# Optimization experiments

Hardware: AMD Instinct MI355X
Metric: run time of the kernel (lower is better)

The kernel has to match this reference:

```python
import jax, jax.numpy as jnp
import numpy as np

# Dims from init_kwargs
B, L, D = 32, 512, 1024
NSEC = 4
SSIZE = D // NSEC          # 256
LATENT = 256
N_TOKENS = 32
BANDS = ((0, 64), (16, 128), (32, 192), (64, 256))
COEF = 0.1


def _dct_mat(N):
    # torch_dct.dct (DCT-II, unnormalized, factor 2): X[k] = 2*sum_n x[n] cos(pi*k*(2n+1)/(2N))
    n = jnp.arange(N, dtype=jnp.float32)
    k = jnp.arange(N, dtype=jnp.float32)[:, None]
    return 2.0 * jnp.cos(jnp.pi * (2.0 * n + 1.0) * k / (2.0 * N))  # [k, n]


def _idct_mat(N):
    # exact inverse of the above (DCT-III form): x[n] = (1/N)*(X[0]/2 + sum_{k>=1} X[k] cos(pi*k*(2n+1)/(2N)))
    k = jnp.arange(N, dtype=jnp.float32)
    n = jnp.arange(N, dtype=jnp.float32)[:, None]
    M = jnp.cos(jnp.pi * k * (2.0 * n + 1.0) / (2.0 * N)) / N
    return M.at[:, 0].set(1.0 / (2.0 * N))  # [n, k]


def setup_inputs() -> dict:
    key = jax.random.key(0)
    k1, k2, k3 = jax.random.split(key, 3)
    encoding = jax.random.normal(k1, (B, L, D), dtype=jnp.float32)
    W = jax.random.normal(k2, (LATENT, SSIZE), dtype=jnp.float32) / np.float32(np.sqrt(SSIZE))
    b = jax.random.normal(k3, (LATENT,), dtype=jnp.float32) * 0.01
    return {"encoding": encoding, "W": W, "b": b}


def reference(encoding, W, b):
    # encoding: [B, L, D] -> [B, L, NSEC, SSIZE]
    enc = encoding.reshape(B, L, NSEC, SSIZE)
    # Literal semantics of the torch code: H = enc[:,:,i] is [B,L,S]; H.T -> [S,L,B];
    # dct/idct act over the LAST axis (= batch), scaling indexes the seq axis.
    C = _dct_mat(B)   # [k, b]
    M = _idct_mat(B)  # [b, k]
    # DCT along batch axis for all sectors at once: [k, L, NSEC, SSIZE]
    Dk = jnp.einsum('kb,blns->klns', C, enc)
    # Per-sector band scaling along the seq axis
    seq = jnp.arange(L)
    mask = jnp.stack(
        [jnp.where((seq < lo) | (seq >= hi), jnp.float32(COEF), jnp.float32(1.0)) for (lo, hi) in BANDS],
        axis=1,
    )  # [L, NSEC]
    Dk = Dk * mask[None, :, :, None]
    # IDCT back along batch axis: [B, L, NSEC, SSIZE]
    filt = jnp.einsum('bk,klns->blns', M, Dk)
    # Linear(SSIZE -> LATENT) + tanh, then keep first N_TOKENS positions
    y = jnp.tanh(jnp.einsum('blns,os->blno', filt, W) + b)
    return y[:, :N_TOKENS]
```

## Files before the change

kernel.cpp:

```cpp
#include <hip/hip_runtime.h>
#include <math.h>

#define LSEQ   512
#define DDIM   1024
#define KDIM   256
#define COLS   256
#define ROWS   4096
#define COEF   0.1f

#define TR    32
#define TC    64
#define BK    64
#define STRA  260
#define STRW  68


__device__ __forceinline__ float tanh_fast(float x) {
    return 1.0f - 2.0f / (__expf(2.0f * x) + 1.0f);
}

__global__ __launch_bounds__(256, 2)
void spectral_gemm_kernel(const float* __restrict__ enc,
                          const float* __restrict__ W,
                          const float* __restrict__ bias,
                          float* __restrict__ out) {
    __shared__ float As[TR * STRA];
    __shared__ float Ws[TC * STRW];

    const int t      = threadIdx.x;
    const int tile_r = blockIdx.x * TR;
    const int tile_c = blockIdx.y * TC;

    const float* srcA = enc + (size_t)(tile_r >> 7) * (size_t)(LSEQ * DDIM)
                            + (size_t)(tile_r & 127) * KDIM;
    #pragma unroll
    for (int it = 0; it < 8; ++it) {
        const int f  = t + it * 256;
        const int r  = f >> 6;
        const int k4 = f & 63;
        const float4 v = *(const float4*)(srcA + (size_t)f * 4);
        *(float4*)&As[r * STRA + k4 * 4] = v;
    }

    const int tx = t & 15;
    const int ty = t >> 4;
    const int r0 = 2 * ty;

    float acc[2][4] = {{0.f,0.f,0.f,0.f},{0.f,0.f,0.f,0.f}};

    for (int p = 0; p < 4; ++p) {
        const int kk = p * BK;

        #pragma unroll
        for (int it = 0; it < 4; ++it) {
            const int o  = (t >> 4) + it * 16;
            const int k4 = t & 15;
            const float4 v =
                *(const float4*)&W[(size_t)(tile_c + o) * KDIM + kk + k4 * 4];
            *(float4*)&Ws[o * STRW + k4 * 4] = v;
        }
        __syncthreads();

        #pragma unroll 8
        for (int k = 0; k < BK; k += 4) {
            const float4 a0 = *(const float4*)&As[r0 * STRA + kk + k];
            const float4 a1 = *(const float4*)&As[(r0 + 1) * STRA + kk + k];
            float4 w[4];
            #pragma unroll
            for (int c = 0; c < 4; ++c)
                w[c] = *(const float4*)&Ws[(tx + 16 * c) * STRW + k];
            #pragma unroll
            for (int c = 0; c < 4; ++c) {
                acc[0][c] += a0.x * w[c].x;
                acc[0][c] += a0.y * w[c].y;
                acc[0][c] += a0.z * w[c].z;
                acc[0][c] += a0.w * w[c].w;
                acc[1][c] += a1.x * w[c].x;
                acc[1][c] += a1.y * w[c].y;
                acc[1][c] += a1.z * w[c].z;
                acc[1][c] += a1.w * w[c].w;
            }
        }
        __syncthreads();
    }

    #pragma unroll
    for (int i = 0; i < 2; ++i) {
        const int row = tile_r + r0 + i;
        const int n = row & 3;
        const int l = (row >> 2) & 31;
        const float scale = (n == 0 || (n == 1 && l >= 16)) ? 1.0f : COEF;
        #pragma unroll
        for (int c = 0; c < 4; ++c) {
            const int col = tile_c + tx + 16 * c;
            out[(size_t)row * COLS + col] = tanh_fast(scale * acc[i][c] + bias[col]);
        }
    }
}

extern "C" void kernel_launch(void* const* d_in, const int* in_sizes, int n_in,
                              void* d_out, int out_size, void* d_ws, size_t ws_size,
                              hipStream_t stream) {
    const float* enc  = (const float*)d_in[0];
    const float* W    = (const float*)d_in[1];
    const float* bias = (const float*)d_in[2];
    float* out = (float*)d_out;

    dim3 grid(ROWS / TR, COLS / TC);
    spectral_gemm_kernel<<<grid, dim3(256), 0, stream>>>(enc, W, bias, out);
}
```

Baseline: 102.9 us.

## Replace LDS-tiled GEMM with register-streamed kernel over pre-transposed weights

Adds a small kernel that transposes W into a float4-interleaved layout in the workspace on every call. The main kernel drops shared-memory tiling: each thread owns one output column for 8 rows and streams A and W straight from global memory, with a one-step software prefetch. All threads in a wavefront read the same A address, so those loads broadcast. The goal is to remove LDS traffic and barriers, at the cost of an extra launch, more L2 reads of W per block, and a prefetch that reads one step past the end of the buffers.

```diff
diff --git a/kernel.cpp b/kernel.cpp
--- a/kernel.cpp
+++ b/kernel.cpp
@@ -8,93 +8,85 @@
 #define ROWS   4096
 #define COEF   0.1f
 
-#define TR    32
-#define TC    64
-#define BK    64
-#define STRA  260
-#define STRW  68
+#define TRB    8
 
 
 __device__ __forceinline__ float tanh_fast(float x) {
     return 1.0f - 2.0f / (__expf(2.0f * x) + 1.0f);
 }
 
+__global__ __launch_bounds__(256, 4)
+void transpose_w4_kernel(const float* __restrict__ W, float* __restrict__ Wt4) {
+    __shared__ float tile[32][33];
+    const int t  = threadIdx.x;
+    const int bx = blockIdx.x;
+    const int by = blockIdx.y;
+    #pragma unroll
+    for (int i = 0; i < 4; ++i) {
+        const int e   = t + i * 256;
+        const int o_l = e >> 5;
+        const int k_l = e & 31;
+        tile[o_l][k_l] = W[(size_t)(by * 32 + o_l) * KDIM + bx * 32 + k_l];
+    }
+    __syncthreads();
+    const int k4_l = t >> 5;
+    const int o_l  = t & 31;
+    float4 v;
+    v.x = tile[o_l][4 * k4_l + 0];
+    v.y = tile[o_l][4 * k4_l + 1];
+    v.z = tile[o_l][4 * k4_l + 2];
+    v.w = tile[o_l][4 * k4_l + 3];
+    *(float4*)&Wt4[(size_t)(bx * 8 + k4_l) * 1024 + (size_t)(by * 32 + o_l) * 4] = v;
+}
+
 __global__ __launch_bounds__(256, 2)
 void spectral_gemm_kernel(const float* __restrict__ enc,
-                          const float* __restrict__ W,
+                          const float* __restrict__ Wt4,
                           const float* __restrict__ bias,
                           float* __restrict__ out) {
-    __shared__ float As[TR * STRA];
-    __shared__ float Ws[TC * STRW];
+    const int t    = threadIdx.x;
+    const int row0 = blockIdx.x * TRB;
 
-    const int t      = threadIdx.x;
-    const int tile_r = blockIdx.x * TR;
-    const int tile_c = blockIdx.y * TC;
+    const float* __restrict__ abase = enc + (size_t)(row0 >> 7) * (size_t)(LSEQ * DDIM)
+                                          + (size_t)(row0 & 127) * KDIM;
+    const float* __restrict__ wbase = Wt4 + (size_t)t * 4;
 
-    const float* srcA = enc + (size_t)(tile_r >> 7) * (size_t)(LSEQ * DDIM)
-                            + (size_t)(tile_r & 127) * KDIM;
+    float acc[TRB] = {0.f, 0.f, 0.f, 0.f, 0.f, 0.f, 0.f, 0.f};
+
+    float4 w = *(const float4*)(wbase);
+    float4 a[TRB];
     #pragma unroll
-    for (int it = 0; it < 8; ++it) {
-        const int f  = t + it * 256;
-        const int r  = f >> 6;
-        const int k4 = f & 63;
-        const float4 v = *(const float4*)(srcA + (size_t)f * 4);
-        *(float4*)&As[r * STRA + k4 * 4] = v;
+    for (int r = 0; r < TRB; ++r)
+        a[r] = *(const float4*)(abase + r * KDIM);
+
+    #pragma unroll 4
+    for (int p = 0; p < 64; ++p) {
+        const float4 wn = *(const float4*)(wbase + (size_t)(p + 1) * 1024);
+        float4 an[TRB];
+        #pragma unroll
+        for (int r = 0; r < TRB; ++r)
+            an[r] = *(const float4*)(abase + r * KDIM + (p + 1) * 4);
+
+        #pragma unroll
+        for (int r = 0; r < TRB; ++r) {
+            acc[r] += a[r].x * w.x;
+            acc[r] += a[r].y * w.y;
+            acc[r] += a[r].z * w.z;
+            acc[r] += a[r].w * w.w;
+        }
+        w = wn;
+        #pragma unroll
+        for (int r = 0; r < TRB; ++r) a[r] = an[r];
     }
 
-    const int tx = t & 15;
-    const int ty = t >> 4;
-    const int r0 = 2 * ty;
-
-    float acc[2][4] = {{0.f,0.f,0.f,0.f},{0.f,0.f,0.f,0.f}};
-
-    for (int p = 0; p < 4; ++p) {
-        const int kk = p * BK;
-
-        #pragma unroll
-        for (int it = 0; it < 4; ++it) {
-            const int o  = (t >> 4) + it * 16;
-            const int k4 = t & 15;
-            const float4 v =
-                *(const float4*)&W[(size_t)(tile_c + o) * KDIM + kk + k4 * 4];
-            *(float4*)&Ws[o * STRW + k4 * 4] = v;
-        }
-        __syncthreads();
-
-        #pragma unroll 8
-        for (int k = 0; k < BK; k += 4) {
-            const float4 a0 = *(const float4*)&As[r0 * STRA + kk + k];
-            const float4 a1 = *(const float4*)&As[(r0 + 1) * STRA + kk + k];
-            float4 w[4];
-            #pragma unroll
-            for (int c = 0; c < 4; ++c)
-                w[c] = *(const float4*)&Ws[(tx + 16 * c) * STRW + k];
-            #pragma unroll
-            for (int c = 0; c < 4; ++c) {
-                acc[0][c] += a0.x * w[c].x;
-                acc[0][c] += a0.y * w[c].y;
-                acc[0][c] += a0.z * w[c].z;
-                acc[0][c] += a0.w * w[c].w;
-                acc[1][c] += a1.x * w[c].x;
-                acc[1][c] += a1.y * w[c].y;
-                acc[1][c] += a1.z * w[c].z;
-                acc[1][c] += a1.w * w[c].w;
-            }
-        }
-        __syncthreads();
-    }
-
+    const float b = bias[t];
     #pragma unroll
-    for (int i = 0; i < 2; ++i) {
-        const int row = tile_r + r0 + i;
+    for (int r = 0; r < TRB; ++r) {
+        const int row = row0 + r;
         const int n = row & 3;
         const int l = (row >> 2) & 31;
         const float scale = (n == 0 || (n == 1 && l >= 16)) ? 1.0f : COEF;
-        #pragma unroll
-        for (int c = 0; c < 4; ++c) {
-            const int col = tile_c + tx + 16 * c;
-            out[(size_t)row * COLS + col] = tanh_fast(scale * acc[i][c] + bias[col]);
-        }
+        out[(size_t)row * COLS + t] = tanh_fast(scale * acc[r] + b);
     }
 }
 
@@ -105,7 +97,8 @@
     const float* W    = (const float*)d_in[1];
     const float* bias = (const float*)d_in[2];
     float* out = (float*)d_out;
+    float* Wt4 = (float*)d_ws;
 
-    dim3 grid(ROWS / TR, COLS / TC);
-    spectral_gemm_kernel<<<grid, dim3(256), 0, stream>>>(enc, W, bias, out);
+    transpose_w4_kernel<<<dim3(8, 8), dim3(256), 0, stream>>>(W, Wt4);
+    spectral_gemm_kernel<<<dim3(ROWS / TRB), dim3(256), 0, stream>>>(enc, Wt4, bias, out);
 }
```

After: 131.5 us. +27.9%, slower.

## Restructure GEMM: wave-uniform W reads from global, XOR-swizzled A tile

Applied to the files above, without the earlier changes.

Changes the block tile from 32x64 to 64x32. W is no longer staged in shared memory. Each wavefront takes 8 output columns, picked wave-uniformly through readfirstlane, and reads W straight from global or cache as broadcast loads. Each lane owns one row of the A tile, which is stored with an XOR swizzle to avoid LDS bank conflicts, and the outputs are written as float4. This removes the per-chunk W staging and barriers, at the cost of a larger 64 KB LDS footprint, which may lower occupancy, and of reading the A tile twice as often relative to W across blocks.

```diff
diff --git a/kernel.cpp b/kernel.cpp
--- a/kernel.cpp
+++ b/kernel.cpp
@@ -8,11 +8,8 @@
 #define ROWS   4096
 #define COEF   0.1f
 
-#define TR    32
-#define TC    64
-#define BK    64
-#define STRA  260
-#define STRW  68
+#define TRB    64
+#define TCB    32
 
 
 __device__ __forceinline__ float tanh_fast(float x) {
@@ -24,78 +21,56 @@
                           const float* __restrict__ W,
                           const float* __restrict__ bias,
                           float* __restrict__ out) {
-    __shared__ float As[TR * STRA];
-    __shared__ float Ws[TC * STRW];
+    __shared__ float As[TRB * KDIM];
 
     const int t      = threadIdx.x;
-    const int tile_r = blockIdx.x * TR;
-    const int tile_c = blockIdx.y * TC;
+    const int tile_r = blockIdx.x * TRB;
+    const int tile_c = blockIdx.y * TCB;
 
     const float* srcA = enc + (size_t)(tile_r >> 7) * (size_t)(LSEQ * DDIM)
                             + (size_t)(tile_r & 127) * KDIM;
     #pragma unroll
-    for (int it = 0; it < 8; ++it) {
-        const int f  = t + it * 256;
+    for (int i = 0; i < 16; ++i) {
+        const int f  = t + i * 256;
         const int r  = f >> 6;
         const int k4 = f & 63;
         const float4 v = *(const float4*)(srcA + (size_t)f * 4);
-        *(float4*)&As[r * STRA + k4 * 4] = v;
+        *(float4*)&As[r * KDIM + ((k4 ^ (r & 15)) << 2)] = v;
+    }
+    __syncthreads();
+
+    const int lane = t & 63;
+    const int cg   = __builtin_amdgcn_readfirstlane(t >> 6);
+    const float* __restrict__ Wp   = W + (size_t)(tile_c + cg * 8) * KDIM;
+    const float* __restrict__ arow = As + lane * KDIM;
+    const int swz = lane & 15;
+
+    float acc[8] = {0.f,0.f,0.f,0.f,0.f,0.f,0.f,0.f};
+
+    #pragma unroll 4
+    for (int p = 0; p < 64; ++p) {
+        const float4 a = *(const float4*)(arow + ((p ^ swz) << 2));
+        #pragma unroll
+        for (int c = 0; c < 8; ++c) {
+            const float4 w = *(const float4*)(Wp + c * KDIM + p * 4);
+            acc[c] += a.x * w.x;
+            acc[c] += a.y * w.y;
+            acc[c] += a.z * w.z;
+            acc[c] += a.w * w.w;
+        }
     }
 
-    const int tx = t & 15;
-    const int ty = t >> 4;
-    const int r0 = 2 * ty;
-
-    float acc[2][4] = {{0.f,0.f,0.f,0.f},{0.f,0.f,0.f,0.f}};
-
-    for (int p = 0; p < 4; ++p) {
-        const int kk = p * BK;
-
-        #pragma unroll
-        for (int it = 0; it < 4; ++it) {
-            const int o  = (t >> 4) + it * 16;
-            const int k4 = t & 15;
-            const float4 v =
-                *(const float4*)&W[(size_t)(tile_c + o) * KDIM + kk + k4 * 4];
-            *(float4*)&Ws[o * STRW + k4 * 4] = v;
-        }
-        __syncthreads();
-
-        #pragma unroll 8
-        for (int k = 0; k < BK; k += 4) {
-            const float4 a0 = *(const float4*)&As[r0 * STRA + kk + k];
-            const float4 a1 = *(const float4*)&As[(r0 + 1) * STRA + kk + k];
-            float4 w[4];
-            #pragma unroll
-            for (int c = 0; c < 4; ++c)
-                w[c] = *(const float4*)&Ws[(tx + 16 * c) * STRW + k];
-            #pragma unroll
-            for (int c = 0; c < 4; ++c) {
-                acc[0][c] += a0.x * w[c].x;
-                acc[0][c] += a0.y * w[c].y;
-                acc[0][c] += a0.z * w[c].z;
-                acc[0][c] += a0.w * w[c].w;
-                acc[1][c] += a1.x * w[c].x;
-                acc[1][c] += a1.y * w[c].y;
-                acc[1][c] += a1.z * w[c].z;
-                acc[1][c] += a1.w * w[c].w;
-            }
-        }
-        __syncthreads();
-    }
-
+    const int row = tile_r + lane;
+    const int n = row & 3;
+    const int l = (row >> 2) & 31;
+    const float scale = (n == 0 || (n == 1 && l >= 16)) ? 1.0f : COEF;
+    float o[8];
     #pragma unroll
-    for (int i = 0; i < 2; ++i) {
-        const int row = tile_r + r0 + i;
-        const int n = row & 3;
-        const int l = (row >> 2) & 31;
-        const float scale = (n == 0 || (n == 1 && l >= 16)) ? 1.0f : COEF;
-        #pragma unroll
-        for (int c = 0; c < 4; ++c) {
-            const int col = tile_c + tx + 16 * c;
-            out[(size_t)row * COLS + col] = tanh_fast(scale * acc[i][c] + bias[col]);
-        }
-    }
+    for (int c = 0; c < 8; ++c)
+        o[c] = tanh_fast(scale * acc[c] + bias[tile_c + cg * 8 + c]);
+    float4* outp = (float4*)(out + (size_t)row * COLS + tile_c + cg * 8);
+    outp[0] = make_float4(o[0], o[1], o[2], o[3]);
+    outp[1] = make_float4(o[4], o[5], o[6], o[7]);
 }
 
 extern "C" void kernel_launch(void* const* d_in, const int* in_sizes, int n_in,
@@ -106,6 +81,6 @@
     const float* bias = (const float*)d_in[2];
     float* out = (float*)d_out;
 
-    dim3 grid(ROWS / TR, COLS / TC);
+    dim3 grid(ROWS / TRB, COLS / TCB);
     spectral_gemm_kernel<<<grid, dim3(256), 0, stream>>>(enc, W, bias, out);
 }
```

Result: slower. 127.1 us (+23.5%).
